# Kernel optimization log

Hardware: AMD Instinct MI355X
Metric: run time of the kernel (lower is better)

Reference implementation:

```python
import jax, jax.numpy as jnp
import numpy as np

DIM = 784
HEADS = 2
DH = DIM // HEADS  # 392
EPS_LN = 1e-5
EPS_L2 = 1e-12


def layer_norm(x, w, b):
    mu = jnp.mean(x, axis=-1, keepdims=True)
    var = jnp.mean(jnp.square(x - mu), axis=-1, keepdims=True)
    return (x - mu) * jax.lax.rsqrt(var + EPS_LN) * w + b


def hardswish(x):
    return x * jnp.clip(x + 3.0, 0.0, 6.0) / 6.0


def l2norm(x):
    n = jnp.sqrt(jnp.sum(jnp.square(x), axis=-1, keepdims=True))
    return x / jnp.maximum(n, EPS_L2)


def setup_inputs() -> dict:
    key = jax.random.key(0)
    ks = jax.random.split(key, 8)
    B, N = 32, 1024
    x = jax.random.normal(ks[0], (B, N, DIM), dtype=jnp.float32)
    s = 0.02
    qkv_w = jax.random.normal(ks[1], (3 * DIM, DIM), dtype=jnp.float32) * s
    qkv_b = jax.random.normal(ks[2], (3 * DIM,), dtype=jnp.float32) * s
    out_w = jax.random.normal(ks[3], (DIM, DIM), dtype=jnp.float32) * s
    out_b = jax.random.normal(ks[4], (DIM,), dtype=jnp.float32) * s
    ffn_w = jax.random.normal(ks[5], (DIM, DIM), dtype=jnp.float32) * s
    ffn_b = jax.random.normal(ks[6], (DIM,), dtype=jnp.float32) * s
    ln_w = jnp.ones((DIM,), dtype=jnp.float32)
    ln_b = jnp.zeros((DIM,), dtype=jnp.float32)
    scale = jnp.ones((HEADS, 1, 1), dtype=jnp.float32) * 0.01
    return {"x": x, "ln_w": ln_w, "ln_b": ln_b, "qkv_w": qkv_w, "qkv_b": qkv_b,
            "scale": scale, "out_w": out_w, "out_b": out_b, "ffn_w": ffn_w, "ffn_b": ffn_b}


def reference(x, ln_w, ln_b, qkv_w, qkv_b, scale, out_w, out_b, ffn_w, ffn_b):
    B, N, _ = x.shape
    h = HEADS
    xn = layer_norm(x, ln_w, ln_b)
    qkv = xn @ qkv_w.T + qkv_b  # [B, N, 3*DIM]
    q, k, v = jnp.split(qkv, 3, axis=-1)
    # 'b n (h d) -> b h n d'
    def to_heads(t):
        return t.reshape(B, N, h, DH).transpose(0, 2, 1, 3)
    q, k, v = to_heads(q), to_heads(k), to_heads(v)
    q, k = l2norm(q), l2norm(k)
    sim = jnp.einsum('bhnd,bhmd->bhnm', q, k) * jnp.sqrt(scale)  # scale [h,1,1] broadcasts
    attn = jax.nn.softmax(sim, axis=-1)
    out = jnp.einsum('bhnm,bhmd->bhnd', attn, v)
    out = out.transpose(0, 2, 1, 3).reshape(B, N, DIM)  # 'b h n d -> b n (h d)'
    out = layer_norm(out, ln_w, ln_b)  # same LayerNorm params reused
    out = hardswish(out)
    out_ffn = hardswish(out @ ffn_w.T + ffn_b)
    return (out + out_ffn) @ out_w.T + out_b
```

## Files before the change

kernel.cpp:

```cpp
#include <hip/hip_runtime.h>

typedef unsigned short u16;
typedef unsigned int u32;
typedef __attribute__((ext_vector_type(4))) float f32x4;
typedef __attribute__((ext_vector_type(8))) short bf16x8;

#define TOK 32768
#define KP  832
#define NKT 13
#define DHP 416
#define DHPV 512
#define NQKV 2560

static __device__ __forceinline__ float bf2f(u16 u){ u32 v = ((u32)u)<<16; return __builtin_bit_cast(float, v); }
static __device__ __forceinline__ u16 f2bf(float f){
  u32 x = __builtin_bit_cast(u32, f);
  u32 r = (x + 0x7fffu + ((x>>16)&1u)) >> 16;
  return (u16)r;
}
static __device__ __forceinline__ void gload16(const void* g, void* l){
  __builtin_amdgcn_global_load_lds((const __attribute__((address_space(1))) void*)g,
                                   (__attribute__((address_space(3))) void*)l, 16, 0, 0);
}
static __device__ __forceinline__ float wave_red_sum(float v){
  #pragma unroll
  for (int o = 32; o > 0; o >>= 1) v += __shfl_xor(v, o, 64);
  return v;
}

__global__ __launch_bounds__(256) void wconv_k(const float* __restrict__ src, u16* __restrict__ dst,
                                               int srcR, long long total){
  long long i = (long long)blockIdx.x*256 + threadIdx.x;
  if (i >= total) return;
  int r = (int)(i / KP), c = (int)(i % KP);
  float v = (r < srcR && c < 784) ? src[(long long)r*784 + c] : 0.f;
  dst[i] = f2bf(v);
}

__global__ __launch_bounds__(256) void ln1_k(const float* __restrict__ x, const float* __restrict__ w,
                                             const float* __restrict__ b, u16* __restrict__ out){
  const int tid = threadIdx.x;
  const long long row = blockIdx.x;
  const float* xr = x + row*784;
  float v[4]; float s = 0.f, ss = 0.f;
  #pragma unroll
  for (int i = 0; i < 4; i++){ int c = tid + i*256; float t = (c < 784) ? xr[c] : 0.f; v[i] = t; s += t; ss += t*t; }
  __shared__ float red[8];
  s = wave_red_sum(s); ss = wave_red_sum(ss);
  if ((tid & 63) == 0){ red[tid>>6] = s; red[4 + (tid>>6)] = ss; }
  __syncthreads();
  float S  = red[0]+red[1]+red[2]+red[3];
  float SS = red[4]+red[5]+red[6]+red[7];
  float mean = S * (1.f/784.f);
  float var  = SS * (1.f/784.f) - mean*mean;
  float rstd = rsqrtf(var + 1e-5f);
  u16* orow = out + row*KP;
  #pragma unroll
  for (int i = 0; i < 4; i++){
    int c = tid + i*256;
    if (c < KP){
      u16 o = 0;
      if (c < 784) o = f2bf((v[i]-mean)*rstd*w[c] + b[c]);
      orow[c] = o;
    }
  }
}

__global__ __launch_bounds__(256) void ln2hs_k(const u16* __restrict__ a, const float* __restrict__ w,
                                               const float* __restrict__ b, u16* __restrict__ out){
  const int tid = threadIdx.x;
  const long long row = blockIdx.x;
  const u16* ar = a + row*784;
  float v[4]; float s = 0.f, ss = 0.f;
  #pragma unroll
  for (int i = 0; i < 4; i++){ int c = tid + i*256; float t = (c < 784) ? bf2f(ar[c]) : 0.f; v[i] = t; s += t; ss += t*t; }
  __shared__ float red[8];
  s = wave_red_sum(s); ss = wave_red_sum(ss);
  if ((tid & 63) == 0){ red[tid>>6] = s; red[4 + (tid>>6)] = ss; }
  __syncthreads();
  float S  = red[0]+red[1]+red[2]+red[3];
  float SS = red[4]+red[5]+red[6]+red[7];
  float mean = S * (1.f/784.f);
  float var  = SS * (1.f/784.f) - mean*mean;
  float rstd = rsqrtf(var + 1e-5f);
  u16* orow = out + row*KP;
  #pragma unroll
  for (int i = 0; i < 4; i++){
    int c = tid + i*256;
    if (c < KP){
      u16 o = 0;
      if (c < 784){
        float y = (v[i]-mean)*rstd*w[c] + b[c];
        y = y * fminf(fmaxf(y + 3.f, 0.f), 6.f) * (1.f/6.f);
        o = f2bf(y);
      }
      orow[c] = o;
    }
  }
}

__global__ __launch_bounds__(256) void l2n_k(u16* __restrict__ Q, u16* __restrict__ Kb,
                                             const float* __restrict__ scale){
  const int lane = threadIdx.x & 63, wv = threadIdx.x >> 6;
  const long long rid = (long long)blockIdx.x*4 + wv;
  const bool isK = rid >= 65536;
  const long long idx = isK ? rid - 65536 : rid;
  u16* base = (isK ? Kb : Q) + idx*DHP;
  uint2 t0 = *(const uint2*)(base + lane*4);
  int ch1 = lane + 64;
  uint2 t1 = (ch1 < 104) ? *(const uint2*)(base + ch1*4) : make_uint2(0u,0u);
  float f0[4], f1[4];
  u32 c0[2] = {t0.x, t0.y}, c1[2] = {t1.x, t1.y};
  #pragma unroll
  for (int j = 0; j < 4; j++){
    f0[j] = bf2f((u16)(c0[j>>1] >> ((j&1)*16)));
    f1[j] = bf2f((u16)(c1[j>>1] >> ((j&1)*16)));
  }
  float ssq = 0.f;
  #pragma unroll
  for (int j = 0; j < 4; j++) ssq += f0[j]*f0[j];
  if (ch1 < 98){
    #pragma unroll
    for (int j = 0; j < 4; j++) ssq += f1[j]*f1[j];
  }
  ssq = wave_red_sum(ssq);
  float fac = 1.f / fmaxf(sqrtf(ssq), 1e-12f);
  if (!isK) fac *= sqrtf(scale[(int)((idx >> 10) & 1)]);
  u32 o0[2], o1[2];
  #pragma unroll
  for (int j = 0; j < 2; j++){
    u16 lo = f2bf(f0[2*j]*fac),   hi = f2bf(f0[2*j+1]*fac);
    o0[j] = (u32)lo | ((u32)hi << 16);
    u16 lo1 = (ch1 < 98) ? f2bf(f1[2*j]*fac)   : (u16)0;
    u16 hi1 = (ch1 < 98) ? f2bf(f1[2*j+1]*fac) : (u16)0;
    o1[j] = (u32)lo1 | ((u32)hi1 << 16);
  }
  *(uint2*)(base + lane*4) = make_uint2(o0[0], o0[1]);
  if (ch1 < 104) *(uint2*)(base + ch1*4) = make_uint2(o1[0], o1[1]);
}

__global__ __launch_bounds__(512, 2) void attn_k(const u16* __restrict__ Qb, const u16* __restrict__ Kb,
    const u16* __restrict__ Vtb, u16* __restrict__ att)
{
  __shared__ u16 smem[40960];
  u16* Pbuf = smem + 24576;

  const int tid = threadIdx.x, lane = tid & 63, wid = tid >> 6;
  const int wq  = wid >> 2, kvw = wid & 3;
  const int dw  = wid >> 2, qw  = wid & 3;

  const int lin = (int)blockIdx.x;
  const int bh = (lin & 7)*8 + (lin >> 6);
  const int qt = (lin >> 3) & 7;

  const u16* Qp = Qb  + ((long long)bh*1024 + (long long)qt*128)*DHP;
  const u16* Kp = Kb  + (long long)bh*1024*DHP;
  const u16* Vp = Vtb + (long long)bh*DHPV*1024;

  const int srow = tid >> 2;
  const int scol = (((tid & 3) ^ ((srow >> 1) & 3)) << 3);
  const int s2   = tid + 512;
  const int r2   = s2 >> 2;
  const int c2   = (((s2 & 3) ^ ((r2 >> 1) & 3)) << 3);

  int offq[4], offk[2], offv[7];
  #pragma unroll
  for (int m = 0; m < 4; m++){
    int r = wq*64 + m*16 + (lane & 15);
    offq[m] = r*32 + ((((lane>>4) ^ (r>>1)) & 3) << 3);
  }
  #pragma unroll
  for (int n = 0; n < 2; n++){
    int r = kvw*32 + n*16 + (lane & 15);
    offk[n] = 4096 + r*32 + ((((lane>>4) ^ (r>>1)) & 3) << 3);
  }
  #pragma unroll
  for (int m = 0; m < 7; m++){
    int r = dw*112 + m*16 + (lane & 15);
    offv[m] = r*32 + ((((lane>>4) ^ (r>>1)) & 3) << 3);
  }

  auto stageA = [&](int ck, int t, int buf){
    u16* rb = smem + buf*8192;
    gload16(Qp + (long long)srow*DHP + t*32 + scol,            rb + tid*8);
    gload16(Kp + (long long)(ck*128 + srow)*DHP + t*32 + scol, rb + 4096 + tid*8);
  };
  auto stageV = [&](int ck, int ms, int buf){
    u16* rb = smem + buf*8192;
    const int h = ms >> 2, s = ms & 3;
    const u16* src = Vp + (long long)(h*224)*1024 + ck*128 + s*32;
    gload16(src + (long long)srow*1024 + scol, rb + tid*8);
    gload16(src + (long long)r2*1024  + c2,   rb + s2*8);
  };

  f32x4 oacc[2][7][2];
  #pragma unroll
  for (int h = 0; h < 2; h++)
    #pragma unroll
    for (int m = 0; m < 7; m++)
      #pragma unroll
      for (int n = 0; n < 2; n++) oacc[h][m][n] = f32x4{0.f,0.f,0.f,0.f};
  float rs_r[16];
  #pragma unroll
  for (int i = 0; i < 16; i++) rs_r[i] = 0.f;

  for (int ck = 0; ck < 8; ++ck){
    stageA(ck, 0, 0); stageA(ck, 1, 1);
    asm volatile("s_waitcnt vmcnt(2)" ::: "memory");
    __builtin_amdgcn_s_barrier();
    f32x4 sacc[4][2];
    #pragma unroll
    for (int m = 0; m < 4; m++)
      #pragma unroll
      for (int n = 0; n < 2; n++) sacc[m][n] = f32x4{0.f,0.f,0.f,0.f};

    for (int t = 0; t < 13; ++t){
      if (t + 2 < 13) stageA(ck, t+2, (t+2)%3);
      const u16* ra = smem + (t%3)*8192;
      bf16x8 aq[4], bk[2];
      #pragma unroll
      for (int m = 0; m < 4; m++) aq[m] = *(const bf16x8*)(ra + offq[m]);
      #pragma unroll
      for (int n = 0; n < 2; n++) bk[n] = *(const bf16x8*)(ra + offk[n]);
      __builtin_amdgcn_s_setprio(1);
      #pragma unroll
      for (int m = 0; m < 4; m++)
        #pragma unroll
        for (int n = 0; n < 2; n++)
          sacc[m][n] = __builtin_amdgcn_mfma_f32_16x16x32_bf16(aq[m], bk[n], sacc[m][n], 0, 0, 0);
      __builtin_amdgcn_s_setprio(0);
      if (t + 2 < 13)      asm volatile("s_waitcnt vmcnt(2)" ::: "memory");
      else if (t + 1 < 13) asm volatile("s_waitcnt vmcnt(0)" ::: "memory");
      if (t + 1 < 13) __builtin_amdgcn_s_barrier();
    }
    __builtin_amdgcn_s_barrier();

    stageV(ck, 0, 0); stageV(ck, 1, 1);
    #pragma unroll
    for (int m = 0; m < 4; m++){
      #pragma unroll
      for (int i = 0; i < 4; i++){
        const int q = wq*64 + m*16 + (lane>>4)*4 + i;
        float a = 0.f;
        #pragma unroll
        for (int n = 0; n < 2; n++){
          const int kv = kvw*32 + n*16 + (lane & 15);
          u16 pb = f2bf(__expf(sacc[m][n][i]));
          Pbuf[q*128 + (((kv>>3) ^ (q&15)) << 3) + (kv&7)] = pb;
          a += bf2f(pb);
        }
        rs_r[m*4+i] += a;
      }
    }
    asm volatile("s_waitcnt vmcnt(2) lgkmcnt(0)" ::: "memory");
    __builtin_amdgcn_s_barrier();

    #pragma unroll
    for (int ms = 0; ms < 8; ++ms){
      if (ms + 2 < 8) stageV(ck, ms+2, (ms+2)%3);
      const u16* vb = smem + (ms%3)*8192;
      const int s = ms & 3;
      const int h = ms >> 2;
      bf16x8 av[7], bp[2];
      #pragma unroll
      for (int m = 0; m < 7; m++) av[m] = *(const bf16x8*)(vb + offv[m]);
      #pragma unroll
      for (int n = 0; n < 2; n++){
        const int q = qw*32 + n*16 + (lane & 15);
        const int cc = s*4 + (lane>>4);
        bp[n] = *(const bf16x8*)(Pbuf + q*128 + ((cc ^ (q&15)) << 3));
      }
      __builtin_amdgcn_s_setprio(1);
      #pragma unroll
      for (int m = 0; m < 7; m++)
        #pragma unroll
        for (int n = 0; n < 2; n++)
          oacc[h][m][n] = __builtin_amdgcn_mfma_f32_16x16x32_bf16(av[m], bp[n], oacc[h][m][n], 0, 0, 0);
      __builtin_amdgcn_s_setprio(0);
      if (ms + 2 < 8)      asm volatile("s_waitcnt vmcnt(2)" ::: "memory");
      else if (ms + 1 < 8) asm volatile("s_waitcnt vmcnt(0)" ::: "memory");
      if (ms + 1 < 8) __builtin_amdgcn_s_barrier();
    }
    __builtin_amdgcn_s_barrier();
  }

  float* rsL = (float*)&smem[0];
  float* rsT = rsL + 512;
  #pragma unroll
  for (int m = 0; m < 4; m++){
    #pragma unroll
    for (int i = 0; i < 4; i++){
      float v = rs_r[m*4+i];
      v += __shfl_xor(v, 1, 64); v += __shfl_xor(v, 2, 64);
      v += __shfl_xor(v, 4, 64); v += __shfl_xor(v, 8, 64);
      if ((lane & 15) == 0) rsL[(wq*64 + m*16 + (lane>>4)*4 + i)*4 + kvw] = v;
    }
  }
  __syncthreads();
  if (tid < 128) rsT[tid] = 1.f/(rsL[tid*4]+rsL[tid*4+1]+rsL[tid*4+2]+rsL[tid*4+3]);
  __syncthreads();
  const int b = bh >> 1, hh = bh & 1;
  #pragma unroll
  for (int h = 0; h < 2; h++){
    #pragma unroll
    for (int n = 0; n < 2; n++){
      const int q = qw*32 + n*16 + (lane & 15);
      const float rinv = rsT[q];
      u16* arw = att + ((long long)(b*1024 + qt*128 + q))*784 + hh*392;
      #pragma unroll
      for (int m = 0; m < 7; m++){
        const int d0 = h*224 + dw*112 + m*16 + (lane>>4)*4;
        if (d0 < 392){
          u16 a0 = f2bf(oacc[h][m][n][0]*rinv), a1 = f2bf(oacc[h][m][n][1]*rinv);
          u16 a2 = f2bf(oacc[h][m][n][2]*rinv), a3 = f2bf(oacc[h][m][n][3]*rinv);
          *(u32*)(arw + d0)     = (u32)a0 | ((u32)a1 << 16);
          *(u32*)(arw + d0 + 2) = (u32)a2 | ((u32)a3 << 16);
        }
      }
    }
  }
}

template<int EPI, int ORDER>
__global__ __launch_bounds__(512, 1) void gemm_k(const u16* __restrict__ Ab, const u16* __restrict__ Bb,
    int lda, int ldb,
    const float* __restrict__ fp0, void* __restrict__ vp1, void* __restrict__ vp2, void* __restrict__ vp3)
{
  __shared__ u16 L[8][8192];
  const int tid = threadIdx.x;
  const int lane = tid & 63;
  const int wid = tid >> 6;
  const int wr = wid >> 2, wc = wid & 3;

  const int gx = gridDim.x, gy = gridDim.y;
  const int nwg = gx*gy;
  int lin = (ORDER == 0) ? ((int)blockIdx.x + gx*(int)blockIdx.y)
                         : ((int)blockIdx.y + gy*(int)blockIdx.x);
  const int q8 = nwg >> 3, r8 = nwg & 7;
  const int xcd = lin & 7, base8 = lin >> 3;
  int wg = (xcd < r8 ? xcd*(q8+1) : r8*(q8+1) + (xcd-r8)*q8) + base8;
  int bx, by;
  if (ORDER == 0){ bx = wg % gx; by = wg / gx; }
  else           { by = wg % gy; bx = wg / gy; }

  const u16* A  = Ab + (long long)by*256*lda;
  const u16* Bp = Bb + (long long)bx*256*ldb;

  const int q1 = tid + 512;
  const int q0c = (((tid & 3) ^ ((tid >> 3) & 3)) << 3);
  const int q1c = (((q1  & 3) ^ ((q1  >> 3) & 3)) << 3);
  const u16* gA0 = A  + (long long)(tid >> 2)*lda + q0c;
  const u16* gA1 = A  + (long long)(q1  >> 2)*lda + q1c;
  const u16* gB0 = Bp + (long long)(tid >> 2)*ldb + q0c;
  const u16* gB1 = Bp + (long long)(q1  >> 2)*ldb + q1c;

  auto stageA = [&](int t, int kh){
    u16* d = &L[(t & 1)*4 + kh][0];
    const int k0 = t*64 + kh*32;
    gload16(gA0 + k0, d + tid*8);
    gload16(gA1 + k0, d + q1*8);
  };
  auto stageB = [&](int t, int kh){
    u16* d = &L[(t & 1)*4 + 2 + kh][0];
    const int k0 = t*64 + kh*32;
    gload16(gB0 + k0, d + tid*8);
    gload16(gB1 + k0, d + q1*8);
  };

  int offa[8], offb[4];
  #pragma unroll
  for (int m = 0; m < 8; m++){
    int row = wr*128 + m*16 + (lane & 15);
    offa[m] = row*32 + ((((lane >> 4) ^ (row >> 1)) & 3) << 3);
  }
  #pragma unroll
  for (int n = 0; n < 4; n++){
    int row = wc*64 + n*16 + (lane & 15);
    offb[n] = row*32 + ((((lane >> 4) ^ (row >> 1)) & 3) << 3);
  }

  f32x4 acc[8][4];
  #pragma unroll
  for (int m = 0; m < 8; m++)
    #pragma unroll
    for (int n = 0; n < 4; n++) acc[m][n] = f32x4{0.f,0.f,0.f,0.f};

  bf16x8 af[4], bf[4];
  auto loadA = [&](int t, int kh, int mh){
    const u16* Lb = &L[(t & 1)*4 + kh][0];
    af[0] = *(const bf16x8*)&Lb[offa[mh*4 + 0]];
    af[1] = *(const bf16x8*)&Lb[offa[mh*4 + 1]];
    af[2] = *(const bf16x8*)&Lb[offa[mh*4 + 2]];
    af[3] = *(const bf16x8*)&Lb[offa[mh*4 + 3]];
  };
  auto loadB = [&](int t, int kh){
    const u16* Lb = &L[(t & 1)*4 + 2 + kh][0];
    bf[0] = *(const bf16x8*)&Lb[offb[0]];
    bf[1] = *(const bf16x8*)&Lb[offb[1]];
    bf[2] = *(const bf16x8*)&Lb[offb[2]];
    bf[3] = *(const bf16x8*)&Lb[offb[3]];
  };

  stageA(0,0); stageB(0,0); stageA(0,1); stageB(0,1); stageA(1,0); stageB(1,0);
  asm volatile("s_waitcnt vmcnt(8)" ::: "memory");
  __builtin_amdgcn_s_barrier();

  for (int t = 0; t < NKT; ++t){
    loadA(t, 0, 0); loadB(t, 0);
    if (t + 1 < NKT) stageA(t + 1, 1);
    __builtin_amdgcn_s_barrier();
    asm volatile("s_waitcnt lgkmcnt(0)" ::: "memory");
    __builtin_amdgcn_sched_barrier(0);
    __builtin_amdgcn_s_setprio(1);
    #pragma unroll
    for (int i = 0; i < 4; i++)
      #pragma unroll
      for (int n = 0; n < 4; n++)
        acc[i][n] = __builtin_amdgcn_mfma_f32_16x16x32_bf16(af[i], bf[n], acc[i][n], 0, 0, 0);
    __builtin_amdgcn_s_setprio(0);
    __builtin_amdgcn_s_barrier();

    loadA(t, 0, 1);
    if (t + 1 < NKT) stageB(t + 1, 1);
    __builtin_amdgcn_s_barrier();
    asm volatile("s_waitcnt lgkmcnt(0)" ::: "memory");
    __builtin_amdgcn_sched_barrier(0);
    __builtin_amdgcn_s_setprio(1);
    #pragma unroll
    for (int i = 0; i < 4; i++)
      #pragma unroll
      for (int n = 0; n < 4; n++)
        acc[4+i][n] = __builtin_amdgcn_mfma_f32_16x16x32_bf16(af[i], bf[n], acc[4+i][n], 0, 0, 0);
    __builtin_amdgcn_s_setprio(0);
    if (t < NKT-1) asm volatile("s_waitcnt vmcnt(8)" ::: "memory");
    else           asm volatile("s_waitcnt vmcnt(0)" ::: "memory");
    __builtin_amdgcn_s_barrier();

    loadA(t, 1, 0); loadB(t, 1);
    if (t + 2 < NKT) stageA(t + 2, 0);
    __builtin_amdgcn_s_barrier();
    asm volatile("s_waitcnt lgkmcnt(0)" ::: "memory");
    __builtin_amdgcn_sched_barrier(0);
    __builtin_amdgcn_s_setprio(1);
    #pragma unroll
    for (int i = 0; i < 4; i++)
      #pragma unroll
      for (int n = 0; n < 4; n++)
        acc[i][n] = __builtin_amdgcn_mfma_f32_16x16x32_bf16(af[i], bf[n], acc[i][n], 0, 0, 0);
    __builtin_amdgcn_s_setprio(0);
    __builtin_amdgcn_s_barrier();

    loadA(t, 1, 1);
    if (t + 2 < NKT) stageB(t + 2, 0);
    __builtin_amdgcn_s_barrier();
    asm volatile("s_waitcnt lgkmcnt(0)" ::: "memory");
    __builtin_amdgcn_sched_barrier(0);
    __builtin_amdgcn_s_setprio(1);
    #pragma unroll
    for (int i = 0; i < 4; i++)
      #pragma unroll
      for (int n = 0; n < 4; n++)
        acc[4+i][n] = __builtin_amdgcn_mfma_f32_16x16x32_bf16(af[i], bf[n], acc[4+i][n], 0, 0, 0);
    __builtin_amdgcn_s_setprio(0);
    if (t < NKT-2)       asm volatile("s_waitcnt vmcnt(8)" ::: "memory");
    else if (t == NKT-2) asm volatile("s_waitcnt vmcnt(4)" ::: "memory");
    if (t < NKT-1) __builtin_amdgcn_s_barrier();
  }

  const int tm = by*256 + wr*128;
  const int tn = bx*256 + wc*64;

  if constexpr (EPI == 0){
    __builtin_amdgcn_s_barrier();
    u16* Qn = (u16*)vp1; u16* Kn = (u16*)vp2; u16* Vt = (u16*)vp3;
    u16* W = &L[wid][0];
    #pragma unroll
    for (int m = 0; m < 8; m++){
      const int grp0 = tm + m*16;
      const int row0 = grp0 + (lane>>4)*4;
      if (grp0 < 1568){
        const float b0 = fp0[row0], b1 = fp0[row0+1], b2 = fp0[row0+2], b3 = fp0[row0+3];
        const int dl = m*16 + (lane>>4)*4;
        #pragma unroll
        for (int n = 0; n < 4; n++){
          const int tok = n*16 + (lane&15);
          const int ad  = tok*128 + (dl ^ ((tok&7)<<3));
          u32 lo = (u32)f2bf(acc[m][n][0]+b0) | ((u32)f2bf(acc[m][n][1]+b1) << 16);
          u32 hi = (u32)f2bf(acc[m][n][2]+b2) | ((u32)f2bf(acc[m][n][3]+b3) << 16);
          *(u32*)(W + ad)     = lo;
          *(u32*)(W + ad + 2) = hi;
        }
      } else if (row0 < 2352){
        const int seg = row0 / 392;
        const int hh = seg & 1;
        const int dd0 = row0 - seg*392;
        const float b0 = fp0[row0], b1 = fp0[row0+1], b2 = fp0[row0+2], b3 = fp0[row0+3];
        #pragma unroll
        for (int n = 0; n < 4; n++){
          const int col = tn + n*16 + (lane&15);
          const int bb = col >> 10, nn = col & 1023;
          const long long vb = ((long long)(bb*2 + hh)*DHPV + dd0)*1024 + nn;
          Vt[vb        ] = f2bf(acc[m][n][0] + b0);
          Vt[vb + 1024 ] = f2bf(acc[m][n][1] + b1);
          Vt[vb + 2048 ] = f2bf(acc[m][n][2] + b2);
          Vt[vb + 3072 ] = f2bf(acc[m][n][3] + b3);
        }
      }
    }
    const int climit = min(16, max(0, (1568 - tm) >> 3));
    if (climit > 0){
      const int c  = lane & 15;
      const int r0 = tm + c*8;
      const int seg = min(r0, 1567) / 392;
      const int hh = seg & 1;
      const int d0 = r0 - seg*392;
      u16* dst0 = (seg < 2) ? Qn : Kn;
      #pragma unroll
      for (int tt = 0; tt < 16; tt++){
        const int tok = tt*4 + (lane>>4);
        bf16x8 vv = *(const bf16x8*)(W + tok*128 + ((c*8) ^ ((tok&7)<<3)));
        if (c < climit){
          const int tg = tn + tok;
          const int bb = tg >> 10, nn = tg & 1023;
          *(bf16x8*)(dst0 + ((long long)((bb*2 + hh)*1024 + nn))*DHP + d0) = vv;
        }
      }
    }
  } else {
    #pragma unroll
    for (int m = 0; m < 8; m++){
      #pragma unroll
      for (int n = 0; n < 4; n++){
        #pragma unroll
        for (int i = 0; i < 4; i++){
          const int row = tm + m*16 + (lane>>4)*4 + i;
          const int col = tn + n*16 + (lane&15);
          float v = acc[m][n][i];
          if constexpr (EPI == 4){
            if (col < KP){
              u16 o = 0;
              if (col < 784){
                float f = v + fp0[col];
                f = f * fminf(fmaxf(f + 3.f, 0.f), 6.f) * (1.f/6.f);
                float hv = bf2f(((const u16*)vp1)[(long long)row*KP + col]);
                o = f2bf(hv + f);
              }
              ((u16*)vp2)[(long long)row*KP + col] = o;
            }
          } else {
            if (col < 784){
              ((float*)vp1)[(long long)row*784 + col] = v + fp0[col];
            }
          }
        }
      }
    }
  }
}

extern "C" void kernel_launch(void* const* d_in, const int* in_sizes, int n_in,
                              void* d_out, int out_size, void* d_ws, size_t ws_size,
                              hipStream_t stream)
{
  const float* x     = (const float*)d_in[0];
  const float* ln_w  = (const float*)d_in[1];
  const float* ln_b  = (const float*)d_in[2];
  const float* qkv_w = (const float*)d_in[3];
  const float* qkv_b = (const float*)d_in[4];
  const float* scale = (const float*)d_in[5];
  const float* out_w = (const float*)d_in[6];
  const float* out_b = (const float*)d_in[7];
  const float* ffn_w = (const float*)d_in[8];
  const float* ffn_b = (const float*)d_in[9];

  char* wsp = (char*)d_ws;
  auto alloc = [&](long long bytes)->char*{ char* p = wsp; wsp += (bytes + 255) & ~255LL; return p; };
  u16* XN   = (u16*)alloc((long long)TOK*KP*2);
  u16* WQKV = (u16*)alloc((long long)NQKV*KP*2);
  u16* WFF  = (u16*)alloc(1024LL*KP*2);
  u16* WO   = (u16*)alloc(1024LL*KP*2);
  u16* QN   = (u16*)alloc(64LL*1024*DHP*2);
  u16* KN   = (u16*)alloc(64LL*1024*DHP*2);
  u16* VT   = (u16*)alloc(64LL*DHPV*1024*2);
  u16* ATT = XN;
  u16* H   = QN;
  u16* S   = KN;
  (void)ws_size; (void)in_sizes; (void)n_in; (void)out_size;

  wconv_k<<<dim3(((long long)NQKV*KP + 255)/256), 256, 0, stream>>>(qkv_w, WQKV, 2352, (long long)NQKV*KP);
  wconv_k<<<dim3((1024*KP + 255)/256), 256, 0, stream>>>(ffn_w, WFF, 784, 1024LL*KP);
  wconv_k<<<dim3((1024*KP + 255)/256), 256, 0, stream>>>(out_w, WO,  784, 1024LL*KP);

  ln1_k<<<dim3(TOK), 256, 0, stream>>>(x, ln_w, ln_b, XN);
  gemm_k<0,0><<<dim3(128, 10, 1), 512, 0, stream>>>(WQKV, XN, KP, KP, qkv_b, QN, KN, VT);
  l2n_k<<<dim3(32768), 256, 0, stream>>>(QN, KN, scale);
  attn_k<<<dim3(512), 512, 0, stream>>>(QN, KN, VT, ATT);
  ln2hs_k<<<dim3(TOK), 256, 0, stream>>>(ATT, ln_w, ln_b, H);
  gemm_k<4,0><<<dim3(4, 128, 1), 512, 0, stream>>>(H, WFF, KP, KP, ffn_b, H, S, nullptr);
  gemm_k<5,0><<<dim3(4, 128, 1), 512, 0, stream>>>(S, WO, KP, KP, out_b, d_out, nullptr, nullptr);
}
```

Baseline: 664.9 us.

## Load Q/K/V MFMA operands directly from global memory instead of LDS staging

Removes the triple-buffered global-to-LDS async staging of Q, K and V tiles in the attention kernel, and each wave now loads its MFMA fragments straight from global memory into registers. LDS is kept only for the P matrix and the row-sum reduction. This drops most barriers and shrinks LDS use, which may raise occupancy. In exchange it loses cross-wave data sharing: Q and K fragments are reloaded by several waves, global loads become strided 16-byte accesses, and latency is no longer hidden by prefetching.

```diff
diff --git a/kernel.cpp b/kernel.cpp
--- a/kernel.cpp
+++ b/kernel.cpp
@@ -142,8 +142,9 @@
 __global__ __launch_bounds__(512, 2) void attn_k(const u16* __restrict__ Qb, const u16* __restrict__ Kb,
     const u16* __restrict__ Vtb, u16* __restrict__ att)
 {
-  __shared__ u16 smem[40960];
-  u16* Pbuf = smem + 24576;
+  __shared__ u16 Pbuf[16384];
+  __shared__ float rsL[128][4];
+  __shared__ float rsT[128];
 
   const int tid = threadIdx.x, lane = tid & 63, wid = tid >> 6;
   const int wq  = wid >> 2, kvw = wid & 3;
@@ -157,41 +158,9 @@
   const u16* Kp = Kb  + (long long)bh*1024*DHP;
   const u16* Vp = Vtb + (long long)bh*DHPV*1024;
 
-  const int srow = tid >> 2;
-  const int scol = (((tid & 3) ^ ((srow >> 1) & 3)) << 3);
-  const int s2   = tid + 512;
-  const int r2   = s2 >> 2;
-  const int c2   = (((s2 & 3) ^ ((r2 >> 1) & 3)) << 3);
-
-  int offq[4], offk[2], offv[7];
-  #pragma unroll
-  for (int m = 0; m < 4; m++){
-    int r = wq*64 + m*16 + (lane & 15);
-    offq[m] = r*32 + ((((lane>>4) ^ (r>>1)) & 3) << 3);
-  }
-  #pragma unroll
-  for (int n = 0; n < 2; n++){
-    int r = kvw*32 + n*16 + (lane & 15);
-    offk[n] = 4096 + r*32 + ((((lane>>4) ^ (r>>1)) & 3) << 3);
-  }
-  #pragma unroll
-  for (int m = 0; m < 7; m++){
-    int r = dw*112 + m*16 + (lane & 15);
-    offv[m] = r*32 + ((((lane>>4) ^ (r>>1)) & 3) << 3);
-  }
-
-  auto stageA = [&](int ck, int t, int buf){
-    u16* rb = smem + buf*8192;
-    gload16(Qp + (long long)srow*DHP + t*32 + scol,            rb + tid*8);
-    gload16(Kp + (long long)(ck*128 + srow)*DHP + t*32 + scol, rb + 4096 + tid*8);
-  };
-  auto stageV = [&](int ck, int ms, int buf){
-    u16* rb = smem + buf*8192;
-    const int h = ms >> 2, s = ms & 3;
-    const u16* src = Vp + (long long)(h*224)*1024 + ck*128 + s*32;
-    gload16(src + (long long)srow*1024 + scol, rb + tid*8);
-    gload16(src + (long long)r2*1024  + c2,   rb + s2*8);
-  };
+  const u16* qbase = Qp + (long long)(wq*64  + (lane&15))*DHP  + (lane>>4)*8;
+  const u16* kbase = Kp + (long long)(kvw*32 + (lane&15))*DHP  + (lane>>4)*8;
+  const u16* vbase = Vp + (long long)(dw*112 + (lane&15))*1024 + (lane>>4)*8;
 
   f32x4 oacc[2][7][2];
   #pragma unroll
@@ -205,23 +174,21 @@
   for (int i = 0; i < 16; i++) rs_r[i] = 0.f;
 
   for (int ck = 0; ck < 8; ++ck){
-    stageA(ck, 0, 0); stageA(ck, 1, 1);
-    asm volatile("s_waitcnt vmcnt(2)" ::: "memory");
-    __builtin_amdgcn_s_barrier();
     f32x4 sacc[4][2];
     #pragma unroll
     for (int m = 0; m < 4; m++)
       #pragma unroll
       for (int n = 0; n < 2; n++) sacc[m][n] = f32x4{0.f,0.f,0.f,0.f};
 
+    #pragma unroll
     for (int t = 0; t < 13; ++t){
-      if (t + 2 < 13) stageA(ck, t+2, (t+2)%3);
-      const u16* ra = smem + (t%3)*8192;
       bf16x8 aq[4], bk[2];
       #pragma unroll
-      for (int m = 0; m < 4; m++) aq[m] = *(const bf16x8*)(ra + offq[m]);
-      #pragma unroll
-      for (int n = 0; n < 2; n++) bk[n] = *(const bf16x8*)(ra + offk[n]);
+      for (int m = 0; m < 4; m++)
+        aq[m] = *(const bf16x8*)(qbase + (long long)(m*16)*DHP + t*32);
+      #pragma unroll
+      for (int n = 0; n < 2; n++)
+        bk[n] = *(const bf16x8*)(kbase + (long long)(ck*128 + n*16)*DHP + t*32);
       __builtin_amdgcn_s_setprio(1);
       #pragma unroll
       for (int m = 0; m < 4; m++)
@@ -229,13 +196,8 @@
         for (int n = 0; n < 2; n++)
           sacc[m][n] = __builtin_amdgcn_mfma_f32_16x16x32_bf16(aq[m], bk[n], sacc[m][n], 0, 0, 0);
       __builtin_amdgcn_s_setprio(0);
-      if (t + 2 < 13)      asm volatile("s_waitcnt vmcnt(2)" ::: "memory");
-      else if (t + 1 < 13) asm volatile("s_waitcnt vmcnt(0)" ::: "memory");
-      if (t + 1 < 13) __builtin_amdgcn_s_barrier();
-    }
-    __builtin_amdgcn_s_barrier();
-
-    stageV(ck, 0, 0); stageV(ck, 1, 1);
+    }
+
     #pragma unroll
     for (int m = 0; m < 4; m++){
       #pragma unroll
@@ -252,18 +214,15 @@
         rs_r[m*4+i] += a;
       }
     }
-    asm volatile("s_waitcnt vmcnt(2) lgkmcnt(0)" ::: "memory");
-    __builtin_amdgcn_s_barrier();
+    __syncthreads();
 
     #pragma unroll
     for (int ms = 0; ms < 8; ++ms){
-      if (ms + 2 < 8) stageV(ck, ms+2, (ms+2)%3);
-      const u16* vb = smem + (ms%3)*8192;
-      const int s = ms & 3;
-      const int h = ms >> 2;
+      const int h = ms >> 2, s = ms & 3;
       bf16x8 av[7], bp[2];
       #pragma unroll
-      for (int m = 0; m < 7; m++) av[m] = *(const bf16x8*)(vb + offv[m]);
+      for (int m = 0; m < 7; m++)
+        av[m] = *(const bf16x8*)(vbase + (long long)(h*224 + m*16)*1024 + ck*128 + s*32);
       #pragma unroll
       for (int n = 0; n < 2; n++){
         const int q = qw*32 + n*16 + (lane & 15);
@@ -277,15 +236,10 @@
         for (int n = 0; n < 2; n++)
           oacc[h][m][n] = __builtin_amdgcn_mfma_f32_16x16x32_bf16(av[m], bp[n], oacc[h][m][n], 0, 0, 0);
       __builtin_amdgcn_s_setprio(0);
-      if (ms + 2 < 8)      asm volatile("s_waitcnt vmcnt(2)" ::: "memory");
-      else if (ms + 1 < 8) asm volatile("s_waitcnt vmcnt(0)" ::: "memory");
-      if (ms + 1 < 8) __builtin_amdgcn_s_barrier();
-    }
-    __builtin_amdgcn_s_barrier();
-  }
-
-  float* rsL = (float*)&smem[0];
-  float* rsT = rsL + 512;
+    }
+    __syncthreads();
+  }
+
   #pragma unroll
   for (int m = 0; m < 4; m++){
     #pragma unroll
@@ -293,11 +247,11 @@
       float v = rs_r[m*4+i];
       v += __shfl_xor(v, 1, 64); v += __shfl_xor(v, 2, 64);
       v += __shfl_xor(v, 4, 64); v += __shfl_xor(v, 8, 64);
-      if ((lane & 15) == 0) rsL[(wq*64 + m*16 + (lane>>4)*4 + i)*4 + kvw] = v;
+      if ((lane & 15) == 0) rsL[wq*64 + m*16 + (lane>>4)*4 + i][kvw] = v;
     }
   }
   __syncthreads();
-  if (tid < 128) rsT[tid] = 1.f/(rsL[tid*4]+rsL[tid*4+1]+rsL[tid*4+2]+rsL[tid*4+3]);
+  if (tid < 128) rsT[tid] = 1.f/(rsL[tid][0]+rsL[tid][1]+rsL[tid][2]+rsL[tid][3]);
   __syncthreads();
   const int b = bh >> 1, hh = bh & 1;
   #pragma unroll
```

Result: slower. 1.146 ms (+72.4%).
